# Optimization experiments

Hardware: AMD Instinct MI355X
Metric: run time of the kernel (lower is better)

## Reference

```python
import jax, jax.numpy as jnp
import numpy as np

EPS = 1e-6  # clamp for arccos domain (matches typical GeodesicLoss eps)


def _random_rotations(key, n):
    # Orthonormalize random matrices into proper rotations (stand-in for
    # the gemmi symmetry operators of 'P 61 2 2', S=12 ops).
    A = jax.random.normal(key, (n, 3, 3), dtype=jnp.float32)
    Q, R = jnp.linalg.qr(A)
    # fix signs so det = +1
    d = jnp.sign(jnp.diagonal(R, axis1=-2, axis2=-1))
    Q = Q * d[:, None, :]
    det = jnp.linalg.det(Q)
    Q = Q.at[:, :, 0].multiply(det[:, None])
    return Q


def setup_inputs() -> dict:
    key = jax.random.key(0)
    k1, k2, k3 = jax.random.split(key, 3)
    B, C, S = 32768, 64, 12
    R_pred = _random_rotations(k1, B * C).reshape(B, C, 3, 3)
    R_gt = _random_rotations(k2, B)
    rot_mats = _random_rotations(k3, S)
    return {"R_pred": R_pred, "R_gt": R_gt, "rot_mats": rot_mats}


def reference(R_pred, R_gt, rot_mats):
    # R_gt_sym[b,s] = rot_mats[s] @ R_gt[b]  -> (B, S, 3, 3)
    R_gt_sym = jnp.einsum('sij,bjk->bsik', rot_mats, R_gt)
    # geodesic loss: arccos((trace(R_pred @ R_gt_sym^T) - 1) / 2)
    # trace(A @ B^T) = sum_ij A_ij * B_ij  -> avoids materializing (B,C,S,3,3)
    tr = jnp.einsum('bcij,bsij->bcs', R_pred, R_gt_sym)
    cos = jnp.clip((tr - 1.0) * 0.5, -1.0 + EPS, 1.0 - EPS)
    all_losses = jnp.arccos(cos)            # (B, C, S)
    min_loss_sym = jnp.min(all_losses, axis=2)   # min over symmetry ops
    best_candidate = jnp.min(min_loss_sym, axis=1)  # min over candidates
    return best_candidate.mean()
```

## Files before the change

kernel.cpp:

```cpp
#include <hip/hip_runtime.h>
#include <math.h>

#define EPS_CLIP 1e-6f
#define WPB 4
#define NWAVES 4

struct F3 { float x, y, z; };

template <int SS>
__global__ __launch_bounds__(256) void sym_loss_kernel(
    const float* __restrict__ R_pred,
    const float* __restrict__ R_gt,
    const float* __restrict__ rot,
    float* __restrict__ partial,
    int S_rt)
{
    const int S    = SS ? SS : S_rt;
    const int tid  = threadIdx.x;
    const int lane = tid & 63;
    const int wid  = tid >> 6;
    const int gw   = __builtin_amdgcn_readfirstlane(blockIdx.x * NWAVES + wid);
    const int b0   = gw * WPB;

    F3 a0, a1, a2;
    {
        const F3* src = reinterpret_cast<const F3*>(R_pred + ((size_t)b0 * 64 + lane) * 9);
        a0 = src[0]; a1 = src[1]; a2 = src[2];
    }

    float lsum = 0.f;

    #pragma unroll
    for (int k = 0; k < WPB; ++k) {
        const int b = __builtin_amdgcn_readfirstlane(b0 + k);

        float p[9] = { a0.x, a0.y, a0.z, a1.x, a1.y, a1.z, a2.x, a2.y, a2.z };

        if (k + 1 < WPB) {
            const F3* src = reinterpret_cast<const F3*>(R_pred + ((size_t)(b + 1) * 64 + lane) * 9);
            a0 = src[0]; a1 = src[1]; a2 = src[2];
        }

        const float* G = R_gt + (size_t)b * 9;
        float g[9];
        #pragma unroll
        for (int e = 0; e < 9; ++e) g[e] = G[e];

        float q[9];
        #pragma unroll
        for (int i = 0; i < 3; ++i)
            #pragma unroll
            for (int j = 0; j < 3; ++j)
                q[i * 3 + j] = fmaf(p[i * 3 + 0], g[j * 3 + 0],
                               fmaf(p[i * 3 + 1], g[j * 3 + 1],
                                    p[i * 3 + 2] * g[j * 3 + 2]));

        float m = -1e30f;
        if (SS) {
            #pragma unroll
            for (int s = 0; s < SS; ++s) {
                const float* Rs = rot + s * 9;
                float tr = 0.f;
                #pragma unroll
                for (int e = 0; e < 9; ++e) tr = fmaf(q[e], Rs[e], tr);
                m = fmaxf(m, tr);
            }
        } else {
            for (int s = 0; s < S; ++s) {
                const float* Rs = rot + s * 9;
                float tr = 0.f;
                #pragma unroll
                for (int e = 0; e < 9; ++e) tr = fmaf(q[e], Rs[e], tr);
                m = fmaxf(m, tr);
            }
        }

        #pragma unroll
        for (int off = 32; off; off >>= 1) m = fmaxf(m, __shfl_xor(m, off));

        if (lane == 0) {
            float cosv = (m - 1.0f) * 0.5f;
            cosv = fminf(fmaxf(cosv, -1.0f + EPS_CLIP), 1.0f - EPS_CLIP);
            lsum += acosf(cosv);
        }
    }

    __shared__ float sLoss[NWAVES];
    if (lane == 0) sLoss[wid] = lsum;
    __syncthreads();
    if (tid == 0) {
        float sum = 0.f;
        #pragma unroll
        for (int i = 0; i < NWAVES; ++i) sum += sLoss[i];
        partial[blockIdx.x] = sum;
    }
}

__global__ __launch_bounds__(1024) void reduce_kernel(
    const float* __restrict__ partial, int n, float* __restrict__ out, float invB)
{
    float sum = 0.f;
    for (int i = threadIdx.x; i < n; i += 1024) sum += partial[i];
    #pragma unroll
    for (int off = 32; off; off >>= 1) sum += __shfl_xor(sum, off);
    __shared__ float ws[16];
    const int w = threadIdx.x >> 6;
    if ((threadIdx.x & 63) == 0) ws[w] = sum;
    __syncthreads();
    if (threadIdx.x == 0) {
        float t = 0.f;
        #pragma unroll
        for (int i = 0; i < 16; ++i) t += ws[i];
        out[0] = t * invB;
    }
}

extern "C" void kernel_launch(void* const* d_in, const int* in_sizes, int n_in,
                              void* d_out, int out_size, void* d_ws, size_t ws_size,
                              hipStream_t stream) {
    const float* R_pred = (const float*)d_in[0];
    const float* R_gt   = (const float*)d_in[1];
    const float* rot    = (const float*)d_in[2];
    float* out = (float*)d_out;

    const int B = in_sizes[1] / 9;
    const int S = in_sizes[2] / 9;
    const int nBlocks = B / (WPB * NWAVES);

    float* partial = (float*)d_ws;

    if (S == 12)
        sym_loss_kernel<12><<<nBlocks, 256, 0, stream>>>(R_pred, R_gt, rot, partial, S);
    else
        sym_loss_kernel<0><<<nBlocks, 256, 0, stream>>>(R_pred, R_gt, rot, partial, S);

    reduce_kernel<<<1, 1024, 0, stream>>>(partial, nBlocks, out, 1.0f / (float)B);
}
```

Before: 21.37 us.

## Fuse final reduction via last-block atomic counter and batch all R_pred loads upfront

Replaces the separate reduce kernel with a last-block-done pattern: each block stores its partial sum, bumps an atomic counter, and the final block sums all partials and writes the mean. Each wave now handles 8 batches instead of 4, and all R_pred loads for those batches are issued up front rather than prefetched one ahead. The per-batch acos on lane 0 is replaced by one parallel acos across lanes, followed by a small shuffle reduction. This removes a kernel launch and raises memory-level parallelism, at the cost of an extra memset, higher register pressure and fewer blocks.

```diff
diff --git a/kernel.cpp b/kernel.cpp
--- a/kernel.cpp
+++ b/kernel.cpp
@@ -2,7 +2,7 @@
 #include <math.h>
 
 #define EPS_CLIP 1e-6f
-#define WPB 4
+#define WPB 8
 #define NWAVES 4
 
 struct F3 { float x, y, z; };
@@ -13,7 +13,9 @@
     const float* __restrict__ R_gt,
     const float* __restrict__ rot,
     float* __restrict__ partial,
-    int S_rt)
+    unsigned int* __restrict__ counter,
+    float* __restrict__ out,
+    int S_rt, float invB)
 {
     const int S    = SS ? SS : S_rt;
     const int tid  = threadIdx.x;
@@ -22,29 +24,26 @@
     const int gw   = __builtin_amdgcn_readfirstlane(blockIdx.x * NWAVES + wid);
     const int b0   = gw * WPB;
 
-    F3 a0, a1, a2;
-    {
-        const F3* src = reinterpret_cast<const F3*>(R_pred + ((size_t)b0 * 64 + lane) * 9);
-        a0 = src[0]; a1 = src[1]; a2 = src[2];
+    F3 A[WPB][3];
+    #pragma unroll
+    for (int k = 0; k < WPB; ++k) {
+        const F3* src = reinterpret_cast<const F3*>(R_pred + ((size_t)(b0 + k) * 64 + lane) * 9);
+        A[k][0] = src[0]; A[k][1] = src[1]; A[k][2] = src[2];
     }
 
-    float lsum = 0.f;
-
+    float mk[WPB];
     #pragma unroll
     for (int k = 0; k < WPB; ++k) {
-        const int b = __builtin_amdgcn_readfirstlane(b0 + k);
-
-        float p[9] = { a0.x, a0.y, a0.z, a1.x, a1.y, a1.z, a2.x, a2.y, a2.z };
-
-        if (k + 1 < WPB) {
-            const F3* src = reinterpret_cast<const F3*>(R_pred + ((size_t)(b + 1) * 64 + lane) * 9);
-            a0 = src[0]; a1 = src[1]; a2 = src[2];
-        }
+        const int b = b0 + k;
 
         const float* G = R_gt + (size_t)b * 9;
         float g[9];
         #pragma unroll
         for (int e = 0; e < 9; ++e) g[e] = G[e];
+
+        const float p[9] = { A[k][0].x, A[k][0].y, A[k][0].z,
+                             A[k][1].x, A[k][1].y, A[k][1].z,
+                             A[k][2].x, A[k][2].y, A[k][2].z };
 
         float q[9];
         #pragma unroll
@@ -77,41 +76,51 @@
 
         #pragma unroll
         for (int off = 32; off; off >>= 1) m = fmaxf(m, __shfl_xor(m, off));
-
-        if (lane == 0) {
-            float cosv = (m - 1.0f) * 0.5f;
-            cosv = fminf(fmaxf(cosv, -1.0f + EPS_CLIP), 1.0f - EPS_CLIP);
-            lsum += acosf(cosv);
-        }
+        mk[k] = m;
     }
 
+    float mv = mk[0];
+    #pragma unroll
+    for (int k = 1; k < WPB; ++k) mv = (lane == k) ? mk[k] : mv;
+    float cosv = (mv - 1.0f) * 0.5f;
+    cosv = fminf(fmaxf(cosv, -1.0f + EPS_CLIP), 1.0f - EPS_CLIP);
+    float a = (lane < WPB) ? acosf(cosv) : 0.0f;
+    #pragma unroll
+    for (int off = 1; off < WPB; off <<= 1) a += __shfl_xor(a, off);
+
     __shared__ float sLoss[NWAVES];
-    if (lane == 0) sLoss[wid] = lsum;
+    if (lane == 0) sLoss[wid] = a;
     __syncthreads();
+
     if (tid == 0) {
+        float bsum = 0.f;
+        #pragma unroll
+        for (int i = 0; i < NWAVES; ++i) bsum += sLoss[i];
+        __hip_atomic_store(&partial[blockIdx.x], bsum,
+                           __ATOMIC_RELAXED, __HIP_MEMORY_SCOPE_AGENT);
+        unsigned prev = __hip_atomic_fetch_add(counter, 1u,
+                           __ATOMIC_ACQ_REL, __HIP_MEMORY_SCOPE_AGENT);
+        sLoss[0] = (prev == gridDim.x - 1) ? 1.0f : 0.0f;
+    }
+    __syncthreads();
+
+    if (sLoss[0] != 0.0f) {
+        const int n = gridDim.x;
         float sum = 0.f;
+        for (int i = tid; i < n; i += 256)
+            sum += __hip_atomic_load(&partial[i],
+                       __ATOMIC_RELAXED, __HIP_MEMORY_SCOPE_AGENT);
         #pragma unroll
-        for (int i = 0; i < NWAVES; ++i) sum += sLoss[i];
-        partial[blockIdx.x] = sum;
-    }
-}
-
-__global__ __launch_bounds__(1024) void reduce_kernel(
-    const float* __restrict__ partial, int n, float* __restrict__ out, float invB)
-{
-    float sum = 0.f;
-    for (int i = threadIdx.x; i < n; i += 1024) sum += partial[i];
-    #pragma unroll
-    for (int off = 32; off; off >>= 1) sum += __shfl_xor(sum, off);
-    __shared__ float ws[16];
-    const int w = threadIdx.x >> 6;
-    if ((threadIdx.x & 63) == 0) ws[w] = sum;
-    __syncthreads();
-    if (threadIdx.x == 0) {
-        float t = 0.f;
-        #pragma unroll
-        for (int i = 0; i < 16; ++i) t += ws[i];
-        out[0] = t * invB;
+        for (int off = 32; off; off >>= 1) sum += __shfl_xor(sum, off);
+        __shared__ float ws[NWAVES];
+        if (lane == 0) ws[wid] = sum;
+        __syncthreads();
+        if (tid == 0) {
+            float t = 0.f;
+            #pragma unroll
+            for (int i = 0; i < NWAVES; ++i) t += ws[i];
+            out[0] = t * invB;
+        }
     }
 }
 
@@ -128,11 +137,14 @@
     const int nBlocks = B / (WPB * NWAVES);
 
     float* partial = (float*)d_ws;
+    unsigned* counter = (unsigned*)((char*)d_ws + (size_t)nBlocks * sizeof(float));
+
+    hipMemsetAsync(counter, 0, sizeof(unsigned), stream);
 
     if (S == 12)
-        sym_loss_kernel<12><<<nBlocks, 256, 0, stream>>>(R_pred, R_gt, rot, partial, S);
+        sym_loss_kernel<12><<<nBlocks, 256, 0, stream>>>(
+            R_pred, R_gt, rot, partial, counter, out, S, 1.0f / (float)B);
     else
-        sym_loss_kernel<0><<<nBlocks, 256, 0, stream>>>(R_pred, R_gt, rot, partial, S);
-
-    reduce_kernel<<<1, 1024, 0, stream>>>(partial, nBlocks, out, 1.0f / (float)B);
+        sym_loss_kernel<0><<<nBlocks, 256, 0, stream>>>(
+            R_pred, R_gt, rot, partial, counter, out, S, 1.0f / (float)B);
 }
```

New measurement: 49.84 us. 133% more time.
